# Performance work log

Hardware: AMD Instinct MI355X
Metric: run time of the kernel (lower is better)

Reference implementation:

```python
import jax, jax.numpy as jnp
import numpy as np

B, C, HC, H, W = 4, 512, 64, 64, 64


def _spectral_norm(Wm, u):
    # one torch-style power iteration; u,v are treated as constants (detached)
    v = Wm.T @ u
    v = v / jnp.maximum(jnp.linalg.norm(v), 1e-12)
    u2 = Wm @ v
    u2 = u2 / jnp.maximum(jnp.linalg.norm(u2), 1e-12)
    u2 = jax.lax.stop_gradient(u2)
    v = jax.lax.stop_gradient(v)
    sigma = u2 @ (Wm @ v)
    return Wm / sigma


def setup_inputs() -> dict:
    key = jax.random.key(0)
    ks = jax.random.split(key, 14)
    return {
        "x": jax.random.normal(ks[0], (B, C, H, W), jnp.float32),
        "Wf": jax.random.normal(ks[1], (HC, C), jnp.float32) * 0.05,
        "bf": jax.random.normal(ks[2], (HC,), jnp.float32) * 0.05,
        "Wg": jax.random.normal(ks[3], (HC, C), jnp.float32) * 0.05,
        "bg": jax.random.normal(ks[4], (HC,), jnp.float32) * 0.05,
        "Wh": jax.random.normal(ks[5], (HC, C), jnp.float32) * 0.05,
        "bh": jax.random.normal(ks[6], (HC,), jnp.float32) * 0.05,
        "Wv": jax.random.normal(ks[7], (C, HC), jnp.float32) * 0.05,
        "bv": jax.random.normal(ks[8], (C,), jnp.float32) * 0.05,
        "uf": jax.random.normal(ks[9], (HC,), jnp.float32),
        "ug": jax.random.normal(ks[10], (HC,), jnp.float32),
        "uh": jax.random.normal(ks[11], (HC,), jnp.float32),
        "uv": jax.random.normal(ks[12], (C,), jnp.float32),
        "gamma": jax.random.normal(ks[13], (1,), jnp.float32),
    }


def reference(x, Wf, bf, Wg, bg, Wh, bh, Wv, bv, uf, ug, uh, uv, gamma):
    nb, nc, imgh, imgw = x.shape
    n = imgh * imgw
    xf = x.reshape(nb, nc, n)  # [B, C, N]
    Wf_sn = _spectral_norm(Wf, uf)
    Wg_sn = _spectral_norm(Wg, ug)
    Wh_sn = _spectral_norm(Wh, uh)
    Wv_sn = _spectral_norm(Wv, uv)
    # 1x1 convs are per-pixel GEMMs
    f = jnp.einsum('kc,bcn->bkn', Wf_sn, xf) + bf[:, None]  # [B, HC, N]
    g = jnp.einsum('kc,bcn->bkn', Wg_sn, xf) + bg[:, None]
    h = jnp.einsum('kc,bcn->bkn', Wh_sn, xf) + bh[:, None]
    s = jnp.einsum('bkn,bkm->bnm', f, g)       # [B, N, N] scores
    beta = jax.nn.softmax(s, axis=-1)
    o = jnp.einsum('bnm,bkm->bkn', beta, h)    # [B, HC, N] (already transposed)
    out = jnp.einsum('ck,bkn->bcn', Wv_sn, o) + bv[:, None]
    out = out.reshape(nb, nc, imgh, imgw)
    return gamma[0] * out + x
```

## Files before the change

### kernel.cpp

```cpp
#include <hip/hip_runtime.h>
#include <hip/hip_bf16.h>

typedef __attribute__((ext_vector_type(8))) short short8;
typedef __attribute__((ext_vector_type(4))) float floatx4;
typedef __attribute__((ext_vector_type(16))) float floatx16;
typedef unsigned short ushortt;

#define LOG2E 1.4426950408889634f

__device__ __forceinline__ float fast_exp2(float x) {
    return __builtin_amdgcn_exp2f(x);
}
__device__ __forceinline__ ushortt f2bf(float f) {
    unsigned int u = __float_as_uint(f);
    u += 0x7fffu + ((u >> 16) & 1u);
    return (ushortt)(u >> 16);
}
__device__ __forceinline__ unsigned int f2bf_pk(float a, float b) {
    float2 t; t.x = a; t.y = b;
    __hip_bfloat162 h = __float22bfloat162_rn(t);
    return *reinterpret_cast<unsigned int*>(&h);
}
__device__ __forceinline__ float bf2f(ushortt h) {
    return __uint_as_float(((unsigned int)h) << 16);
}

__device__ __forceinline__ float block_sum(float v, float* red) {
    #pragma unroll
    for (int off = 32; off > 0; off >>= 1) v += __shfl_down(v, off);
    int wid = threadIdx.x >> 6, ln = threadIdx.x & 63;
    __syncthreads();
    if (ln == 0) red[wid] = v;
    __syncthreads();
    return red[0] + red[1] + red[2] + red[3];
}

__global__ __launch_bounds__(256) void sigma_kernel(
    const float* __restrict__ Wf, const float* __restrict__ uf,
    const float* __restrict__ Wg, const float* __restrict__ ug,
    const float* __restrict__ Wh, const float* __restrict__ uh,
    const float* __restrict__ Wv, const float* __restrict__ uv,
    float* __restrict__ sig,
    ushortt* __restrict__ wqkv, ushortt* __restrict__ wvb) {
    __shared__ float tv[512];
    __shared__ float tvp[256];
    __shared__ float zpart[256];
    __shared__ float red[4];
    __shared__ float ssig;
    const int mat = blockIdx.x, tid = threadIdx.x;

    if (mat < 3) {
        const float* W = (mat == 0) ? Wf : ((mat == 1) ? Wg : Wh);
        const float* u = (mat == 0) ? uf : ((mat == 1) ? ug : uh);
        {
            float s0 = 0.f, s1 = 0.f;
            #pragma unroll 8
            for (int r = 0; r < 64; ++r) {
                float ur = u[r];
                s0 += W[r * 512 + tid] * ur;
                s1 += W[r * 512 + tid + 256] * ur;
            }
            tv[tid] = s0;
            tv[tid + 256] = s1;
        }
        __syncthreads();
        float p = tv[tid] * tv[tid] + tv[tid + 256] * tv[tid + 256];
        float nt2 = block_sum(p, red);
        float nt = fmaxf(sqrtf(nt2), 1e-12f);
        {
            int r = tid & 63, qq = tid >> 6;
            const float* Wr = W + r * 512 + qq * 128;
            const float* tq = tv + qq * 128;
            float part = 0.f;
            #pragma unroll 16
            for (int c = 0; c < 128; ++c) part += Wr[c] * tq[c];
            zpart[tid] = part;
        }
        __syncthreads();
        if (tid < 64) {
            float z = zpart[tid] + zpart[tid + 64] + zpart[tid + 128] + zpart[tid + 192];
            z = z * z;
            #pragma unroll
            for (int off = 32; off > 0; off >>= 1) z += __shfl_xor(z, off);
            if (tid == 0) {
                float sg0 = sqrtf(z) / nt;
                sig[mat] = sg0;
                ssig = sg0;
            }
        }
        __syncthreads();
        float inv = 1.0f / ssig;
        const float4* W4 = reinterpret_cast<const float4*>(W);
        unsigned int* dst = reinterpret_cast<unsigned int*>(wqkv + mat * 32768);
        for (int i = tid; i < 8192; i += 256) {
            float4 wv = W4[i];
            dst[2 * i]     = f2bf_pk(wv.x * inv, wv.y * inv);
            dst[2 * i + 1] = f2bf_pk(wv.z * inv, wv.w * inv);
        }
    } else {
        const float* W = Wv; const float* u = uv;
        {
            int c = tid & 63, rs = tid >> 6;
            float s0 = 0.f;
            #pragma unroll 8
            for (int r = rs * 128; r < rs * 128 + 128; ++r) s0 += W[r * 64 + c] * u[r];
            tvp[tid] = s0;
        }
        __syncthreads();
        if (tid < 64) tv[tid] = tvp[tid] + tvp[tid + 64] + tvp[tid + 128] + tvp[tid + 192];
        __syncthreads();
        float t = (tid < 64) ? tv[tid] : 0.f;
        float nt2 = block_sum(t * t, red);
        float nt = fmaxf(sqrtf(nt2), 1e-12f);
        float sg3;
        {
            const float* w1 = W + (size_t)tid * 64;
            const float* w2 = W + (size_t)(tid + 256) * 64;
            float z1 = 0.f, z2 = 0.f;
            #pragma unroll 8
            for (int c = 0; c < 64; ++c) {
                float tc = tv[c];
                z1 += w1[c] * tc;
                z2 += w2[c] * tc;
            }
            float zp = z1 * z1 + z2 * z2;
            float z2t = block_sum(zp, red);
            sg3 = sqrtf(z2t) / nt;
            if (tid == 0) sig[3] = sg3;
        }
        float inv = 1.0f / sg3;
        const float4* W4 = reinterpret_cast<const float4*>(W);
        unsigned int* dst = reinterpret_cast<unsigned int*>(wvb);
        for (int i = tid; i < 8192; i += 256) {
            float4 wv = W4[i];
            dst[2 * i]     = f2bf_pk(wv.x * inv, wv.y * inv);
            dst[2 * i + 1] = f2bf_pk(wv.z * inv, wv.w * inv);
        }
    }
}

__global__ __launch_bounds__(256, 3) void qkv_kernel(
    const float* __restrict__ x, const ushortt* __restrict__ wqkv,
    const float* __restrict__ bfv, const float* __restrict__ bgv,
    const float* __restrict__ bhv,
    ushortt* __restrict__ Qb, ushortt* __restrict__ Kb, ushortt* __restrict__ Vt) {
    __shared__ unsigned int xs[2048];
    const int tid = threadIdx.x;
    const int n0 = blockIdx.x * 32, b = blockIdx.y;
    const int lane = tid & 63, w = tid >> 6;
    const int strip = w & 1, ksel = w >> 1;
    const int q = lane >> 4, l15 = lane & 15;
    const int sn = tid & 31, sg = tid >> 5;

    floatx4 acc[6];
    #pragma unroll
    for (int kt = 0; kt < 6; ++kt) acc[kt] = (floatx4){0.f, 0.f, 0.f, 0.f};

    const float* xb = x + ((size_t)b * 512) * 4096 + n0 + sn;
    const int sslot = sn * 32 + ((sg ^ (sn & 7)) << 2);
    float2 pre[4];
    #pragma unroll
    for (int i = 0; i < 4; ++i) {
        int c = sg * 8 + 2 * i;
        pre[i].x = xb[(size_t)c * 4096];
        pre[i].y = xb[(size_t)(c + 1) * 4096];
    }
    {
        uint4 pk;
        pk.x = f2bf_pk(pre[0].x, pre[0].y);
        pk.y = f2bf_pk(pre[1].x, pre[1].y);
        pk.z = f2bf_pk(pre[2].x, pre[2].y);
        pk.w = f2bf_pk(pre[3].x, pre[3].y);
        *reinterpret_cast<uint4*>(&xs[sslot]) = pk;
    }
    #pragma unroll
    for (int i = 0; i < 4; ++i) {
        int c = 64 + sg * 8 + 2 * i;
        pre[i].x = xb[(size_t)c * 4096];
        pre[i].y = xb[(size_t)(c + 1) * 4096];
    }

    for (int it = 0; it < 8; ++it) {
        __syncthreads();
        if (it < 7) {
            uint4 pk;
            pk.x = f2bf_pk(pre[0].x, pre[0].y);
            pk.y = f2bf_pk(pre[1].x, pre[1].y);
            pk.z = f2bf_pk(pre[2].x, pre[2].y);
            pk.w = f2bf_pk(pre[3].x, pre[3].y);
            *reinterpret_cast<uint4*>(&xs[(((it + 1) & 1) << 10) + sslot]) = pk;
        }
        if (it < 6) {
            #pragma unroll
            for (int i = 0; i < 4; ++i) {
                int c = (it + 2) * 64 + sg * 8 + 2 * i;
                pre[i].x = xb[(size_t)c * 4096];
                pre[i].y = xb[(size_t)(c + 1) * 4096];
            }
        }
        const int c0 = it * 64;
        const unsigned int* xr = &xs[((it & 1) << 10) + (16 * strip + l15) * 32];
        #pragma unroll
        for (int kc = 0; kc < 2; ++kc) {
            union { uint4 v; short8 s8; } af;
            af.v = *reinterpret_cast<const uint4*>(&xr[((4 * kc + q) ^ (l15 & 7)) << 2]);
            #pragma unroll
            for (int kt = 0; kt < 6; ++kt) {
                short8 bb = *reinterpret_cast<const short8*>(
                    &wqkv[(size_t)(ksel * 96 + kt * 16 + l15) * 512 + c0 + kc * 32 + q * 8]);
                acc[kt] = __builtin_amdgcn_mfma_f32_16x16x32_bf16(af.s8, bb, acc[kt], 0, 0, 0);
            }
        }
    }

    const int nloc = n0 + 16 * strip + 4 * q;
    if (ksel == 0) {
        #pragma unroll
        for (int kt = 0; kt < 4; ++kt) {
            int k = kt * 16 + l15;
            float bb = bfv[k];
            #pragma unroll
            for (int r = 0; r < 4; ++r)
                Qb[((size_t)b * 4096 + nloc + r) * 64 + k] = f2bf((acc[kt][r] + bb) * LOG2E);
        }
        #pragma unroll
        for (int kt = 4; kt < 6; ++kt) {
            int k = (kt - 4) * 16 + l15;
            float bb = bgv[k];
            #pragma unroll
            for (int r = 0; r < 4; ++r)
                Kb[((size_t)b * 4096 + nloc + r) * 64 + k] = f2bf(acc[kt][r] + bb);
        }
    } else {
        #pragma unroll
        for (int kt = 0; kt < 2; ++kt) {
            int k = 32 + kt * 16 + l15;
            float bb = bgv[k];
            #pragma unroll
            for (int r = 0; r < 4; ++r)
                Kb[((size_t)b * 4096 + nloc + r) * 64 + k] = f2bf(acc[kt][r] + bb);
        }
    }
    __syncthreads();
    if (ksel == 1) {
        #pragma unroll
        for (int kt = 2; kt < 6; ++kt) {
            int d = (kt - 2) * 16 + l15;
            float bb = bhv[d];
            int base = d * 17 + 8 * strip + 2 * q;
            xs[base]     = f2bf_pk(acc[kt][0] + bb, acc[kt][1] + bb);
            xs[base + 1] = f2bf_pk(acc[kt][2] + bb, acc[kt][3] + bb);
        }
    }
    __syncthreads();
    {
        int d = tid >> 2, sgg = tid & 3;
        uint4 vv;
        vv.x = xs[d * 17 + sgg * 4 + 0]; vv.y = xs[d * 17 + sgg * 4 + 1];
        vv.z = xs[d * 17 + sgg * 4 + 2]; vv.w = xs[d * 17 + sgg * 4 + 3];
        *reinterpret_cast<uint4*>(&Vt[((size_t)b * 64 + d) * 4096 + n0 + sgg * 8]) = vv;
    }
}

__global__ __launch_bounds__(256, 3) void attn_kernel(
    const ushortt* __restrict__ Qb, const ushortt* __restrict__ Kb,
    const ushortt* __restrict__ Vt, ushortt* __restrict__ Opart,
    float2* __restrict__ ml, ushortt* __restrict__ Ob, int KB) {
    __shared__ unsigned int smem[8448];
    const int tid = threadIdx.x;
    int n0, b, s;
    if (gridDim.z == 4) {
        int fid = blockIdx.x + 64 * blockIdx.y + 256 * blockIdx.z;
        int xcd = fid & 7, idx = fid >> 3;
        b = xcd >> 1;
        int within = ((xcd & 1) << 7) + idx;
        s = within >> 6;
        n0 = (within & 63) * 64;
    } else {
        n0 = blockIdx.x * 64; b = blockIdx.y; s = blockIdx.z;
    }
    const int lane = tid & 63, w = tid >> 6;
    const int qh = w & 1, kh = w >> 1;
    const int l31 = lane & 31, h = lane >> 5;

    const ushortt* Kg = Kb + (size_t)b * 4096 * 64;
    const ushortt* Vg = Vt + (size_t)b * 64 * 4096;

    short8 bq[4];
    {
        const ushortt* Qg = Qb + ((size_t)b * 4096 + n0 + 32 * qh + l31) * 64;
        #pragma unroll
        for (int kc = 0; kc < 4; ++kc)
            bq[kc] = *reinterpret_cast<const short8*>(Qg + kc * 16 + 8 * h);
    }

    floatx16 ot0 = {}, ot1 = {};
    float m_i = -1e30f, l_i = 0.f;

    const int row = tid >> 2, seg = tid & 3;
    const int kbeg = s * KB, kend = kbeg + KB;
    const int rsw = row & 7;
    const int ws0 = row * 32 + ((((2 * seg)) ^ rsw) << 2);
    const int ws1 = row * 32 + ((((2 * seg + 1)) ^ rsw) << 2);

    uint4 ck0, ck1, cv0, cv1;
    {
        int nb = kbeg * 64;
        const ushortt* kp = Kg + (size_t)(nb + row) * 64 + seg * 16;
        ck0 = *reinterpret_cast<const uint4*>(kp);
        ck1 = *reinterpret_cast<const uint4*>(kp + 8);
        const ushortt* vp = Vg + (size_t)row * 4096 + nb + seg * 16;
        cv0 = *reinterpret_cast<const uint4*>(vp);
        cv1 = *reinterpret_cast<const uint4*>(vp + 8);
    }
    *reinterpret_cast<uint4*>(&smem[ws0]) = ck0;
    *reinterpret_cast<uint4*>(&smem[ws1]) = ck1;
    *reinterpret_cast<uint4*>(&smem[2048 + ws0]) = cv0;
    *reinterpret_cast<uint4*>(&smem[2048 + ws1]) = cv1;
    if (kbeg + 1 < kend) {
        int nb = (kbeg + 1) * 64;
        const ushortt* kp = Kg + (size_t)(nb + row) * 64 + seg * 16;
        ck0 = *reinterpret_cast<const uint4*>(kp);
        ck1 = *reinterpret_cast<const uint4*>(kp + 8);
        const ushortt* vp = Vg + (size_t)row * 4096 + nb + seg * 16;
        cv0 = *reinterpret_cast<const uint4*>(vp);
        cv1 = *reinterpret_cast<const uint4*>(vp + 8);
    }

    for (int kb = kbeg; kb < kend; ++kb) {
        const int cur = (kb - kbeg) & 1;
        const unsigned int rb = cur ? 4096u : 0u;
        const unsigned int wbs = cur ? 0u : 4096u;
        __syncthreads();
        if (kb + 1 < kend) {
            *reinterpret_cast<uint4*>(&smem[wbs + ws0]) = ck0;
            *reinterpret_cast<uint4*>(&smem[wbs + ws1]) = ck1;
            *reinterpret_cast<uint4*>(&smem[wbs + 2048 + ws0]) = cv0;
            *reinterpret_cast<uint4*>(&smem[wbs + 2048 + ws1]) = cv1;
        }
        if (kb + 2 < kend) {
            int nb = (kb + 2) * 64;
            const ushortt* kp = Kg + (size_t)(nb + row) * 64 + seg * 16;
            ck0 = *reinterpret_cast<const uint4*>(kp);
            ck1 = *reinterpret_cast<const uint4*>(kp + 8);
            const ushortt* vp = Vg + (size_t)row * 4096 + nb + seg * 16;
            cv0 = *reinterpret_cast<const uint4*>(vp);
            cv1 = *reinterpret_cast<const uint4*>(vp + 8);
        }

        floatx16 st = {};
        const unsigned int* kr = &smem[rb + (32 * kh + l31) * 32];
        const int esw = l31 & 7;
        __builtin_amdgcn_s_setprio(1);
        #pragma unroll
        for (int kc = 0; kc < 4; ++kc) {
            union { uint4 v; short8 s8; } af;
            af.v = *reinterpret_cast<const uint4*>(&kr[((2 * kc + h) ^ esw) << 2]);
            st = __builtin_amdgcn_mfma_f32_32x32x16_bf16(af.s8, bq[kc], st, 0, 0, 0);
        }
        __builtin_amdgcn_s_setprio(0);

        float mx = fmaxf(fmaxf(fmaxf(st[0], st[1]), fmaxf(st[2], st[3])),
                         fmaxf(fmaxf(st[4], st[5]), fmaxf(st[6], st[7])));
        float mx2 = fmaxf(fmaxf(fmaxf(st[8], st[9]), fmaxf(st[10], st[11])),
                          fmaxf(fmaxf(st[12], st[13]), fmaxf(st[14], st[15])));
        mx = fmaxf(mx, mx2);
        mx = fmaxf(mx, __shfl_xor(mx, 32));
        if (!__all(mx <= m_i + 8.f)) {
            float mn = fmaxf(m_i, mx);
            float alpha = fast_exp2(m_i - mn);
            m_i = mn;
            l_i *= alpha;
            #pragma unroll
            for (int r = 0; r < 16; ++r) { ot0[r] *= alpha; ot1[r] *= alpha; }
        }
        float p[16], rs = 0.f;
        #pragma unroll
        for (int r = 0; r < 16; ++r) { p[r] = fast_exp2(st[r] - m_i); rs += p[r]; }
        rs += __shfl_xor(rs, 32);
        l_i += rs;

        unsigned int pk[8], sp[8];
        #pragma unroll
        for (int i = 0; i < 8; ++i) pk[i] = f2bf_pk(p[2 * i], p[2 * i + 1]);
        #pragma unroll
        for (int i = 0; i < 8; ++i) sp[i] = (unsigned int)__shfl_xor((int)pk[i], 32);
        union { unsigned int u[4]; short8 s8; } pb0, pb1;
        pb0.u[0] = h ? sp[2] : pk[0]; pb0.u[1] = h ? sp[3] : pk[1];
        pb0.u[2] = h ? pk[2] : sp[0]; pb0.u[3] = h ? pk[3] : sp[1];
        pb1.u[0] = h ? sp[6] : pk[4]; pb1.u[1] = h ? sp[7] : pk[5];
        pb1.u[2] = h ? pk[6] : sp[4]; pb1.u[3] = h ? pk[7] : sp[5];

        const unsigned int* vr0 = &smem[rb + 2048 + l31 * 32];
        const unsigned int* vr1 = &smem[rb + 2048 + (32 + l31) * 32];
        __builtin_amdgcn_s_setprio(1);
        #pragma unroll
        for (int c = 0; c < 2; ++c) {
            union { uint4 v; short8 s8; } af;
            af.v = *reinterpret_cast<const uint4*>(&vr0[((4 * kh + 2 * c + h) ^ esw) << 2]);
            ot0 = __builtin_amdgcn_mfma_f32_32x32x16_bf16(af.s8, c ? pb1.s8 : pb0.s8, ot0, 0, 0, 0);
            af.v = *reinterpret_cast<const uint4*>(&vr1[((4 * kh + 2 * c + h) ^ esw) << 2]);
            ot1 = __builtin_amdgcn_mfma_f32_32x32x16_bf16(af.s8, c ? pb1.s8 : pb0.s8, ot1, 0, 0, 0);
        }
        __builtin_amdgcn_s_setprio(0);
    }

    __syncthreads();
    if (h == 0) {
        smem[8192 + w * 32 + l31] = __float_as_uint(m_i);
        smem[8320 + w * 32 + l31] = __float_as_uint(l_i);
    }
    __syncthreads();
    int pw = 2 * (1 - kh) + qh;
    float m2 = __uint_as_float(smem[8192 + pw * 32 + l31]);
    float l2 = __uint_as_float(smem[8320 + pw * 32 + l31]);
    float mstar = fmaxf(m_i, m2);
    float wself = fast_exp2(m_i - mstar);
    float w2 = fast_exp2(m2 - mstar);
    float lm = wself * l_i + w2 * l2;
    float sc = (gridDim.z == 1) ? (wself / lm) : wself;
    if (gridDim.z > 1 && kh == 0 && h == 0) {
        float2 v; v.x = mstar; v.y = lm;
        ml[((size_t)s * 4 + b) * 4096 + n0 + 32 * qh + l31] = v;
    }
    float* om = reinterpret_cast<float*>(smem);
    if (kh == 0) {
        #pragma unroll
        for (int r = 0; r < 16; ++r) {
            int d0 = (r & 3) + 8 * (r >> 2) + 4 * h;
            om[(32 * qh + l31) * 65 + d0] = sc * ot0[r];
            om[(32 * qh + l31) * 65 + 32 + d0] = sc * ot1[r];
        }
    }
    __syncthreads();
    if (kh == 1) {
        #pragma unroll
        for (int r = 0; r < 16; ++r) {
            int d0 = (r & 3) + 8 * (r >> 2) + 4 * h;
            om[(32 * qh + l31) * 65 + d0] += sc * ot0[r];
            om[(32 * qh + l31) * 65 + 32 + d0] += sc * ot1[r];
        }
    }
    __syncthreads();
    {
        int qq = tid >> 2, dsg = tid & 3;
        unsigned int pkk[8];
        #pragma unroll
        for (int j = 0; j < 8; ++j)
            pkk[j] = f2bf_pk(om[qq * 65 + dsg * 16 + 2 * j], om[qq * 65 + dsg * 16 + 2 * j + 1]);
        ushortt* base = (gridDim.z == 1)
            ? (Ob + ((size_t)b * 4096 + n0) * 64)
            : (Opart + (((size_t)s * 4 + b) * 4096 + n0) * 64);
        uint4* d4 = reinterpret_cast<uint4*>(base + (size_t)qq * 64 + dsg * 16);
        uint4 o0; o0.x = pkk[0]; o0.y = pkk[1]; o0.z = pkk[2]; o0.w = pkk[3];
        uint4 o1; o1.x = pkk[4]; o1.y = pkk[5]; o1.z = pkk[6]; o1.w = pkk[7];
        d4[0] = o0; d4[1] = o1;
    }
}

__global__ __launch_bounds__(256, 3) void proj_kernel(
    const ushortt* __restrict__ Opart, const float2* __restrict__ ml,
    const ushortt* __restrict__ Ob, const ushortt* __restrict__ wvb,
    const float* __restrict__ bv, const float* __restrict__ gamma,
    const float* __restrict__ x, float* __restrict__ out, int S) {
    __shared__ ushortt ol[32 * 72];
    const int tid = threadIdx.x;
    const int n0 = blockIdx.x * 32, b = blockIdx.y;

    {
        int row = tid >> 3, t8 = tid & 7;
        int rg = n0 + row;
        if (S == 1) {
            uint4 v = *reinterpret_cast<const uint4*>(
                Ob + ((size_t)b * 4096 + rg) * 64 + t8 * 8);
            *reinterpret_cast<uint4*>(&ol[row * 72 + t8 * 8]) = v;
        } else {
            float2 mls[4];
            float m = -1e30f;
            #pragma unroll 4
            for (int s = 0; s < 4; ++s) {
                mls[s] = ml[((size_t)s * 4 + b) * 4096 + rg];
                m = fmaxf(m, mls[s].x);
            }
            float wgt[4], denom = 0.f;
            #pragma unroll 4
            for (int s = 0; s < 4; ++s) {
                wgt[s] = fast_exp2(mls[s].x - m);
                denom += wgt[s] * mls[s].y;
            }
            float inv = 1.0f / denom;
            float acc[8];
            #pragma unroll
            for (int j = 0; j < 8; ++j) acc[j] = 0.f;
            #pragma unroll 4
            for (int s = 0; s < 4; ++s) {
                union { uint4 v; ushortt hh[8]; } u;
                u.v = *reinterpret_cast<const uint4*>(
                    Opart + (((size_t)s * 4 + b) * 4096 + rg) * 64 + t8 * 8);
                float ww = wgt[s];
                #pragma unroll
                for (int j = 0; j < 8; ++j) acc[j] += ww * bf2f(u.hh[j]);
            }
            uint4 v;
            v.x = f2bf_pk(acc[0] * inv, acc[1] * inv);
            v.y = f2bf_pk(acc[2] * inv, acc[3] * inv);
            v.z = f2bf_pk(acc[4] * inv, acc[5] * inv);
            v.w = f2bf_pk(acc[6] * inv, acc[7] * inv);
            *reinterpret_cast<uint4*>(&ol[row * 72 + t8 * 8]) = v;
        }
    }
    __syncthreads();

    const int w = tid >> 6, lane = tid & 63, q = lane >> 4, l15 = lane & 15;
    short8 bfr[2][2];
    #pragma unroll
    for (int u = 0; u < 2; ++u)
        #pragma unroll
        for (int kc = 0; kc < 2; ++kc)
            bfr[u][kc] = *reinterpret_cast<const short8*>(
                &ol[(16 * u + l15) * 72 + 32 * kc + q * 8]);

    floatx4 acc[8][2];
    #pragma unroll
    for (int t = 0; t < 8; ++t)
        #pragma unroll
        for (int u = 0; u < 2; ++u) acc[t][u] = (floatx4){0.f, 0.f, 0.f, 0.f};

    const int cw = w * 128;
    #pragma unroll
    for (int t = 0; t < 8; ++t) {
        short8 a0 = *reinterpret_cast<const short8*>(
            &wvb[(size_t)(cw + 16 * t + l15) * 64 + q * 8]);
        short8 a1 = *reinterpret_cast<const short8*>(
            &wvb[(size_t)(cw + 16 * t + l15) * 64 + 32 + q * 8]);
        #pragma unroll
        for (int u = 0; u < 2; ++u) {
            acc[t][u] = __builtin_amdgcn_mfma_f32_16x16x32_bf16(a0, bfr[u][0], acc[t][u], 0, 0, 0);
            acc[t][u] = __builtin_amdgcn_mfma_f32_16x16x32_bf16(a1, bfr[u][1], acc[t][u], 0, 0, 0);
        }
    }

    float gm = gamma[0];
    #pragma unroll
    for (int t = 0; t < 8; ++t) {
        #pragma unroll
        for (int r = 0; r < 4; ++r) {
            int c = cw + 16 * t + 4 * q + r;
            float bb = bv[c];
            #pragma unroll
            for (int u = 0; u < 2; ++u) {
                int n = n0 + 16 * u + l15;
                size_t idx = ((size_t)(b * 512 + c)) * 4096 + n;
                out[idx] = gm * (acc[t][u][r] + bb) + x[idx];
            }
        }
    }
}

extern "C" void kernel_launch(void* const* d_in, const int* in_sizes, int n_in,
                              void* d_out, int out_size, void* d_ws, size_t ws_size,
                              hipStream_t stream) {
    const float* x   = (const float*)d_in[0];
    const float* Wf  = (const float*)d_in[1];
    const float* bf_ = (const float*)d_in[2];
    const float* Wg  = (const float*)d_in[3];
    const float* bg_ = (const float*)d_in[4];
    const float* Wh  = (const float*)d_in[5];
    const float* bh_ = (const float*)d_in[6];
    const float* Wv  = (const float*)d_in[7];
    const float* bv_ = (const float*)d_in[8];
    const float* uf  = (const float*)d_in[9];
    const float* ug  = (const float*)d_in[10];
    const float* uh  = (const float*)d_in[11];
    const float* uv  = (const float*)d_in[12];
    const float* gm  = (const float*)d_in[13];
    float* out = (float*)d_out;

    char* ws = (char*)d_ws;
    float*   sig   = (float*)ws;
    ushortt* wqkv  = (ushortt*)(ws + 256);
    ushortt* wvb   = (ushortt*)(ws + 196864);
    ushortt* Qb    = (ushortt*)(ws + 262400);
    ushortt* Kb    = (ushortt*)(ws + 2359552);
    ushortt* Vt    = (ushortt*)(ws + 4456704);
    ushortt* Ob    = (ushortt*)(ws + 6553856);
    float2*  ml    = (float2*)(ws + 8651008);
    ushortt* Opart = (ushortt*)(ws + 9175296);

    int S = (ws_size >= (size_t)17563904) ? 4 : 1;

    sigma_kernel<<<4, 256, 0, stream>>>(Wf, uf, Wg, ug, Wh, uh, Wv, uv, sig, wqkv, wvb);
    qkv_kernel<<<dim3(128, 4), 256, 0, stream>>>(x, wqkv, bf_, bg_, bh_, Qb, Kb, Vt);
    attn_kernel<<<dim3(64, 4, S), 256, 0, stream>>>(Qb, Kb, Vt, Opart, ml, Ob, 64 / S);
    proj_kernel<<<dim3(128, 4), 256, 0, stream>>>(Opart, ml, Ob, wvb, bv_, gm, x, out, S);
}
```

Baseline: 187.1 us.

## Fuse all four stages into one cooperative persistent kernel with grid syncs

Refactors the sigma, QKV, attention and projection kernels into device bodies and adds a cooperative 512-block fused kernel that runs them back to back, separated by grid.sync(). In the fused path attention uses a split of 2 over keys instead of 4, with KB=32, and the projection merges 2 partials. The aim is to remove launch gaps and inter-kernel drain/fill between the stages. In exchange, 508 of the 512 blocks idle during the sigma stage, the grid barriers cost time, attention parallelism per block drops, and the kernel is limited to 2 blocks per CU.

Measured after the change: 193.7 us. 1.04x slower.

```diff
diff --git a/kernel.cpp b/kernel.cpp
--- a/kernel.cpp
+++ b/kernel.cpp
@@ -1,5 +1,8 @@
 #include <hip/hip_runtime.h>
 #include <hip/hip_bf16.h>
+#include <hip/hip_cooperative_groups.h>
+
+namespace cg = cooperative_groups;
 
 typedef __attribute__((ext_vector_type(8))) short short8;
 typedef __attribute__((ext_vector_type(4))) float floatx4;
@@ -35,19 +38,21 @@
     return red[0] + red[1] + red[2] + red[3];
 }
 
-__global__ __launch_bounds__(256) void sigma_kernel(
+
+__device__ __forceinline__ void sigma_body(
+    unsigned int* smem_u, int mat,
     const float* __restrict__ Wf, const float* __restrict__ uf,
     const float* __restrict__ Wg, const float* __restrict__ ug,
     const float* __restrict__ Wh, const float* __restrict__ uh,
     const float* __restrict__ Wv, const float* __restrict__ uv,
     float* __restrict__ sig,
     ushortt* __restrict__ wqkv, ushortt* __restrict__ wvb) {
-    __shared__ float tv[512];
-    __shared__ float tvp[256];
-    __shared__ float zpart[256];
-    __shared__ float red[4];
-    __shared__ float ssig;
-    const int mat = blockIdx.x, tid = threadIdx.x;
+    float* tv    = reinterpret_cast<float*>(smem_u);
+    float* tvp   = tv + 512;
+    float* zpart = tvp + 256;
+    float* red   = zpart + 256;
+    float* ssigp = red + 4;
+    const int tid = threadIdx.x;
 
     if (mat < 3) {
         const float* W = (mat == 0) ? Wf : ((mat == 1) ? Wg : Wh);
@@ -85,11 +90,11 @@
             if (tid == 0) {
                 float sg0 = sqrtf(z) / nt;
                 sig[mat] = sg0;
-                ssig = sg0;
+                ssigp[0] = sg0;
             }
         }
         __syncthreads();
-        float inv = 1.0f / ssig;
+        float inv = 1.0f / ssigp[0];
         const float4* W4 = reinterpret_cast<const float4*>(W);
         unsigned int* dst = reinterpret_cast<unsigned int*>(wqkv + mat * 32768);
         for (int i = tid; i < 8192; i += 256) {
@@ -139,14 +144,13 @@
     }
 }
 
-__global__ __launch_bounds__(256, 3) void qkv_kernel(
+__device__ __forceinline__ void qkv_body(
+    unsigned int* xs, int n0, int b,
     const float* __restrict__ x, const ushortt* __restrict__ wqkv,
     const float* __restrict__ bfv, const float* __restrict__ bgv,
     const float* __restrict__ bhv,
     ushortt* __restrict__ Qb, ushortt* __restrict__ Kb, ushortt* __restrict__ Vt) {
-    __shared__ unsigned int xs[2048];
     const int tid = threadIdx.x;
-    const int n0 = blockIdx.x * 32, b = blockIdx.y;
     const int lane = tid & 63, w = tid >> 6;
     const int strip = w & 1, ksel = w >> 1;
     const int q = lane >> 4, l15 = lane & 15;
@@ -262,23 +266,12 @@
     }
 }
 
-__global__ __launch_bounds__(256, 3) void attn_kernel(
+__device__ __forceinline__ void attn_body(
+    unsigned int* smem, int n0, int b, int s, int KB, bool partial,
     const ushortt* __restrict__ Qb, const ushortt* __restrict__ Kb,
     const ushortt* __restrict__ Vt, ushortt* __restrict__ Opart,
-    float2* __restrict__ ml, ushortt* __restrict__ Ob, int KB) {
-    __shared__ unsigned int smem[8448];
+    float2* __restrict__ ml, ushortt* __restrict__ Ob) {
     const int tid = threadIdx.x;
-    int n0, b, s;
-    if (gridDim.z == 4) {
-        int fid = blockIdx.x + 64 * blockIdx.y + 256 * blockIdx.z;
-        int xcd = fid & 7, idx = fid >> 3;
-        b = xcd >> 1;
-        int within = ((xcd & 1) << 7) + idx;
-        s = within >> 6;
-        n0 = (within & 63) * 64;
-    } else {
-        n0 = blockIdx.x * 64; b = blockIdx.y; s = blockIdx.z;
-    }
     const int lane = tid & 63, w = tid >> 6;
     const int qh = w & 1, kh = w >> 1;
     const int l31 = lane & 31, h = lane >> 5;
@@ -418,8 +411,8 @@
     float wself = fast_exp2(m_i - mstar);
     float w2 = fast_exp2(m2 - mstar);
     float lm = wself * l_i + w2 * l2;
-    float sc = (gridDim.z == 1) ? (wself / lm) : wself;
-    if (gridDim.z > 1 && kh == 0 && h == 0) {
+    float sc = partial ? wself : (wself / lm);
+    if (partial && kh == 0 && h == 0) {
         float2 v; v.x = mstar; v.y = lm;
         ml[((size_t)s * 4 + b) * 4096 + n0 + 32 * qh + l31] = v;
     }
@@ -448,7 +441,7 @@
         #pragma unroll
         for (int j = 0; j < 8; ++j)
             pkk[j] = f2bf_pk(om[qq * 65 + dsg * 16 + 2 * j], om[qq * 65 + dsg * 16 + 2 * j + 1]);
-        ushortt* base = (gridDim.z == 1)
+        ushortt* base = (!partial)
             ? (Ob + ((size_t)b * 4096 + n0) * 64)
             : (Opart + (((size_t)s * 4 + b) * 4096 + n0) * 64);
         uint4* d4 = reinterpret_cast<uint4*>(base + (size_t)qq * 64 + dsg * 16);
@@ -458,14 +451,14 @@
     }
 }
 
-__global__ __launch_bounds__(256, 3) void proj_kernel(
+template <int S>
+__device__ __forceinline__ void proj_body(
+    ushortt* ol, int n0, int b,
     const ushortt* __restrict__ Opart, const float2* __restrict__ ml,
     const ushortt* __restrict__ Ob, const ushortt* __restrict__ wvb,
     const float* __restrict__ bv, const float* __restrict__ gamma,
-    const float* __restrict__ x, float* __restrict__ out, int S) {
-    __shared__ ushortt ol[32 * 72];
+    const float* __restrict__ x, float* __restrict__ out) {
     const int tid = threadIdx.x;
-    const int n0 = blockIdx.x * 32, b = blockIdx.y;
 
     {
         int row = tid >> 3, t8 = tid & 7;
@@ -475,29 +468,29 @@
                 Ob + ((size_t)b * 4096 + rg) * 64 + t8 * 8);
             *reinterpret_cast<uint4*>(&ol[row * 72 + t8 * 8]) = v;
         } else {
-            float2 mls[4];
+            float2 mls[S];
             float m = -1e30f;
-            #pragma unroll 4
-            for (int s = 0; s < 4; ++s) {
-                mls[s] = ml[((size_t)s * 4 + b) * 4096 + rg];
-                m = fmaxf(m, mls[s].x);
-            }
-            float wgt[4], denom = 0.f;
-            #pragma unroll 4
-            for (int s = 0; s < 4; ++s) {
-                wgt[s] = fast_exp2(mls[s].x - m);
-                denom += wgt[s] * mls[s].y;
+            #pragma unroll
+            for (int s2 = 0; s2 < S; ++s2) {
+                mls[s2] = ml[((size_t)s2 * 4 + b) * 4096 + rg];
+                m = fmaxf(m, mls[s2].x);
+            }
+            float wgt[S], denom = 0.f;
+            #pragma unroll
+            for (int s2 = 0; s2 < S; ++s2) {
+                wgt[s2] = fast_exp2(mls[s2].x - m);
+                denom += wgt[s2] * mls[s2].y;
             }
             float inv = 1.0f / denom;
             float acc[8];
             #pragma unroll
             for (int j = 0; j < 8; ++j) acc[j] = 0.f;
-            #pragma unroll 4
-            for (int s = 0; s < 4; ++s) {
+            #pragma unroll
+            for (int s2 = 0; s2 < S; ++s2) {
                 union { uint4 v; ushortt hh[8]; } u;
                 u.v = *reinterpret_cast<const uint4*>(
-                    Opart + (((size_t)s * 4 + b) * 4096 + rg) * 64 + t8 * 8);
-                float ww = wgt[s];
+                    Opart + (((size_t)s2 * 4 + b) * 4096 + rg) * 64 + t8 * 8);
+                float ww = wgt[s2];
                 #pragma unroll
                 for (int j = 0; j < 8; ++j) acc[j] += ww * bf2f(u.hh[j]);
             }
@@ -555,6 +548,87 @@
             }
         }
     }
+}
+
+__global__ __launch_bounds__(256) void sigma_kernel(
+    const float* Wf, const float* uf, const float* Wg, const float* ug,
+    const float* Wh, const float* uh, const float* Wv, const float* uv,
+    float* sig, ushortt* wqkv, ushortt* wvb) {
+    __shared__ unsigned int smem[1056];
+    sigma_body(smem, blockIdx.x, Wf, uf, Wg, ug, Wh, uh, Wv, uv, sig, wqkv, wvb);
+}
+
+__global__ __launch_bounds__(256, 3) void qkv_kernel(
+    const float* x, const ushortt* wqkv,
+    const float* bfv, const float* bgv, const float* bhv,
+    ushortt* Qb, ushortt* Kb, ushortt* Vt) {
+    __shared__ unsigned int xs[2048];
+    qkv_body(xs, blockIdx.x * 32, blockIdx.y, x, wqkv, bfv, bgv, bhv, Qb, Kb, Vt);
+}
+
+__global__ __launch_bounds__(256, 3) void attn_kernel(
+    const ushortt* Qb, const ushortt* Kb, const ushortt* Vt,
+    ushortt* Opart, float2* ml, ushortt* Ob, int KB) {
+    __shared__ unsigned int smem[8448];
+    int n0, b, s;
+    if (gridDim.z == 4) {
+        int fid = blockIdx.x + 64 * blockIdx.y + 256 * blockIdx.z;
+        int xcd = fid & 7, idx = fid >> 3;
+        b = xcd >> 1;
+        int within = ((xcd & 1) << 7) + idx;
+        s = within >> 6;
+        n0 = (within & 63) * 64;
+    } else {
+        n0 = blockIdx.x * 64; b = blockIdx.y; s = blockIdx.z;
+    }
+    attn_body(smem, n0, b, s, KB, gridDim.z > 1, Qb, Kb, Vt, Opart, ml, Ob);
+}
+
+__global__ __launch_bounds__(256, 3) void proj_kernel(
+    const ushortt* Opart, const float2* ml, const ushortt* Ob,
+    const ushortt* wvb, const float* bv, const float* gamma,
+    const float* x, float* out, int S) {
+    __shared__ ushortt ol[32 * 72];
+    if (S == 1)
+        proj_body<1>(ol, blockIdx.x * 32, blockIdx.y, Opart, ml, Ob, wvb, bv, gamma, x, out);
+    else
+        proj_body<4>(ol, blockIdx.x * 32, blockIdx.y, Opart, ml, Ob, wvb, bv, gamma, x, out);
+}
+
+__global__ __launch_bounds__(256, 2) void fused_kernel(
+    const float* x, const float* Wf, const float* bfv, const float* Wg,
+    const float* bgv, const float* Wh, const float* bhv, const float* Wv,
+    const float* bvv, const float* uf, const float* ug, const float* uh,
+    const float* uv, const float* gamma, float* out,
+    float* sig, ushortt* wqkv, ushortt* wvb,
+    ushortt* Qb, ushortt* Kb, ushortt* Vt, ushortt* Ob,
+    float2* ml, ushortt* Opart) {
+    __shared__ unsigned int smem[8448];
+    cg::grid_group grid = cg::this_grid();
+    const int fid = blockIdx.x;
+
+    if (fid < 4)
+        sigma_body(smem, fid, Wf, uf, Wg, ug, Wh, uh, Wv, uv, sig, wqkv, wvb);
+    __threadfence();
+    grid.sync();
+
+    qkv_body(smem, (fid & 127) * 32, fid >> 7, x, wqkv, bfv, bgv, bhv, Qb, Kb, Vt);
+    __threadfence();
+    grid.sync();
+
+    {
+        int xcd = fid & 7, idx = fid >> 3;
+        int b = xcd >> 1;
+        int within = ((xcd & 1) << 6) + idx;
+        int s = within >> 6;
+        int n0 = (within & 63) * 64;
+        attn_body(smem, n0, b, s, 32, true, Qb, Kb, Vt, Opart, ml, Ob);
+    }
+    __threadfence();
+    grid.sync();
+
+    proj_body<2>(reinterpret_cast<ushortt*>(smem), (fid & 127) * 32, fid >> 7,
+                 Opart, ml, Ob, wvb, bvv, gamma, x, out);
 }
 
 extern "C" void kernel_launch(void* const* d_in, const int* in_sizes, int n_in,
@@ -589,8 +663,37 @@
 
     int S = (ws_size >= (size_t)17563904) ? 4 : 1;
 
-    sigma_kernel<<<4, 256, 0, stream>>>(Wf, uf, Wg, ug, Wh, uh, Wv, uv, sig, wqkv, wvb);
-    qkv_kernel<<<dim3(128, 4), 256, 0, stream>>>(x, wqkv, bf_, bg_, bh_, Qb, Kb, Vt);
-    attn_kernel<<<dim3(64, 4, S), 256, 0, stream>>>(Qb, Kb, Vt, Opart, ml, Ob, 64 / S);
-    proj_kernel<<<dim3(128, 4), 256, 0, stream>>>(Opart, ml, Ob, wvb, bv_, gm, x, out, S);
-}
+    static int coop_ok = -1;
+    if (coop_ok < 0) {
+        int dev = 0;
+        (void)hipGetDevice(&dev);
+        int supp = 0;
+        (void)hipDeviceGetAttribute(&supp, hipDeviceAttributeCooperativeLaunch, dev);
+        int nCU = 0;
+        (void)hipDeviceGetAttribute(&nCU, hipDeviceAttributeMultiprocessorCount, dev);
+        int maxb = 0;
+        (void)hipOccupancyMaxActiveBlocksPerMultiprocessor(&maxb, fused_kernel, 256, 0);
+        coop_ok = (supp && (long)maxb * (long)nCU >= 512) ? 1 : 0;
+    }
+
+    bool coop_done = false;
+    if (coop_ok == 1 && S == 4) {
+        void* args[] = {
+            (void*)&x,  (void*)&Wf, (void*)&bf_, (void*)&Wg, (void*)&bg_,
+            (void*)&Wh, (void*)&bh_, (void*)&Wv, (void*)&bv_, (void*)&uf,
+            (void*)&ug, (void*)&uh, (void*)&uv, (void*)&gm, (void*)&out,
+            (void*)&sig, (void*)&wqkv, (void*)&wvb, (void*)&Qb, (void*)&Kb,
+            (void*)&Vt, (void*)&Ob, (void*)&ml, (void*)&Opart};
+        hipError_t e = hipLaunchCooperativeKernel(
+            reinterpret_cast<void*>(fused_kernel), dim3(512), dim3(256),
+            args, 0, stream);
+        coop_done = (e == hipSuccess);
+    }
+
+    if (!coop_done) {
+        sigma_kernel<<<4, 256, 0, stream>>>(Wf, uf, Wg, ug, Wh, uh, Wv, uv, sig, wqkv, wvb);
+        qkv_kernel<<<dim3(128, 4), 256, 0, stream>>>(x, wqkv, bf_, bg_, bh_, Qb, Kb, Vt);
+        attn_kernel<<<dim3(64, 4, S), 256, 0, stream>>>(Qb, Kb, Vt, Opart, ml, Ob, 64 / S);
+        proj_kernel<<<dim3(128, 4), 256, 0, stream>>>(Opart, ml, Ob, wvb, bv_, gm, x, out, S);
+    }
+}
```
